# Performance work log

Measured on AMD Instinct MI355X. Metric: run time of the kernel, lower is better.

## Reference

```python
import jax, jax.numpy as jnp
import numpy as np

NEG_INF = -9e15  # matches the torch fill value


def setup_inputs() -> dict:
    key = jax.random.key(0)
    k1, k2, k3 = jax.random.split(key, 3)
    N, IN_F, OUT_F, C = 8192, 512, 64, 2
    x = jax.random.normal(k1, (N, IN_F), dtype=jnp.float32)
    W = jax.random.normal(k2, (OUT_F, IN_F), dtype=jnp.float32) * (1.0 / np.sqrt(IN_F))
    attention_raw = jax.random.normal(k3, (C * N, N), dtype=jnp.float32)
    return {"x": x, "W": W, "attention_raw": attention_raw, "k": 32}


def reference(x, W, attention_raw, k):
    # h = self.linear(input), bias=False
    h = x @ W.T  # [N, OUT_F]
    N, OUT_F = x.shape[0], W.shape[0]
    R = attention_raw.shape[0]  # C * N
    C = R // N

    # torch.topk(attention, k, dim=1); fill_(-9e15); scatter_ topk values back
    vals, idx = jax.lax.top_k(attention_raw, k)  # [R, k]
    rows = jnp.arange(R)[:, None]
    att = jnp.full_like(attention_raw, NEG_INF).at[rows, idx].set(vals)

    # row softmax; masked entries underflow to exactly 0 -> k-sparse rows
    att = jax.nn.softmax(att, axis=1)
    # dropout skipped (eval mode / deterministic reference)

    # spmm(nzidx, att[nzidx], N*C, N, h) == att @ h (zeros contribute nothing)
    h_prime = att @ h  # [C*N, OUT_F]

    # concat=True path: [C, N, F] -> [N, C, F] -> [N, C*F]
    out = h_prime.reshape(C, N, OUT_F).transpose(1, 0, 2).reshape(N, C * OUT_F)
    return out, att
```

## Files before the change

kernel.cpp:

```cpp
#include <hip/hip_runtime.h>

typedef unsigned int uint;
typedef unsigned short u16;
typedef unsigned long long u64;
typedef float v4f __attribute__((ext_vector_type(4)));

#define N_NODES 8192
#define IN_F    512
#define OUT_F   64
#define CHEADS  2
#define ROWS    (N_NODES * CHEADS)
#define ROW_LEN N_NODES
#define BLK     256
#define PER_TH  (ROW_LEN / BLK)
#define VCHUNKS (PER_TH / 4)
#define CAND_CAP 2048
#define SEL_CAP  64

__device__ __forceinline__ float bits_to_float(uint u) {
    union { uint u; float f; } cv; cv.u = u; return cv.f;
}
__device__ __forceinline__ uint float_to_bits(float f) {
    union { uint u; float f; } cv; cv.f = f; return cv.u;
}
__device__ __forceinline__ uint sortable32(uint u) {
    return u ^ ((u & 0x80000000u) ? 0xFFFFFFFFu : 0x80000000u);
}
__device__ __forceinline__ uint unsortable32(uint s) {
    return (s & 0x80000000u) ? (s ^ 0x80000000u) : ~s;
}
__device__ __forceinline__ float key_to_val(uint key) {
    return bits_to_float(unsortable32(key));
}

__device__ __forceinline__ int decode_k(const void* p) {
    int ki = *(const int*)p;
    if (ki >= 1 && ki <= ROW_LEN) return ki;
    {
        uint b = *(const u16*)p;
        float f = bits_to_float(b << 16);
        int kf = (int)f;
        if (f == (float)kf && kf >= 1 && kf <= ROW_LEN) return kf;
    }
    {
        float g = *(const float*)p;
        int kg = (int)g;
        if (g == (float)kg && kg >= 1 && kg <= ROW_LEN) return kg;
    }
    return 32;
}

__device__ __forceinline__ uint bitonic_desc_u32(uint v, const int lane) {
    #pragma unroll
    for (int size = 2; size <= 64; size <<= 1) {
        #pragma unroll
        for (int stride = size >> 1; stride > 0; stride >>= 1) {
            const uint pv = (uint)__shfl_xor((int)v, stride, 64);
            const bool takeMax = (((lane & stride) != 0) == ((lane & size) != 0));
            v = takeMax ? (v >= pv ? v : pv) : (v <= pv ? v : pv);
        }
    }
    return v;
}

__device__ __forceinline__ u64 bitonic_desc_u64(u64 v, const int lane) {
    #pragma unroll
    for (int size = 2; size <= 64; size <<= 1) {
        #pragma unroll
        for (int stride = size >> 1; stride > 0; stride >>= 1) {
            const u64 pv = __shfl_xor(v, stride, 64);
            const bool takeMax = (((lane & stride) != 0) == ((lane & size) != 0));
            v = takeMax ? (v >= pv ? v : pv) : (v <= pv ? v : pv);
        }
    }
    return v;
}

#define HM    32
#define HK    128
#define XS_LD 132

__global__ __launch_bounds__(256) void h_kernel(
    const float* __restrict__ x, const float* __restrict__ W, float* __restrict__ hbuf)
{
    __shared__ float x_s[HM * XS_LD];
    __shared__ float w_s[OUT_F * XS_LD];
    const int tid = threadIdx.x;
    const int n0  = blockIdx.x * HM;
    const int r   = tid & 15;
    const int fb  = (tid >> 4) << 2;

    float a00 = 0.f, a01 = 0.f, a02 = 0.f, a03 = 0.f;
    float a10 = 0.f, a11 = 0.f, a12 = 0.f, a13 = 0.f;

    for (int c = 0; c < IN_F; c += HK) {
        #pragma unroll
        for (int j = 0; j < 4; ++j) {
            const int id  = tid + 256 * j;
            const int row = id >> 5;
            const int c4  = id & 31;
            float4 v = *reinterpret_cast<const float4*>(x + (size_t)(n0 + row) * IN_F + c + 4 * c4);
            *reinterpret_cast<float4*>(&x_s[row * XS_LD + 4 * c4]) = v;
        }
        #pragma unroll
        for (int j = 0; j < 8; ++j) {
            const int id  = tid + 256 * j;
            const int row = id >> 5;
            const int c4  = id & 31;
            float4 v = *reinterpret_cast<const float4*>(W + (size_t)row * IN_F + c + 4 * c4);
            *reinterpret_cast<float4*>(&w_s[row * XS_LD + 4 * c4]) = v;
        }
        __syncthreads();

        #pragma unroll 4
        for (int k4 = 0; k4 < HK / 4; ++k4) {
            const float4 x0 = *reinterpret_cast<const float4*>(&x_s[r * XS_LD + 4 * k4]);
            const float4 x1 = *reinterpret_cast<const float4*>(&x_s[(r + 16) * XS_LD + 4 * k4]);
            const float4 w0 = *reinterpret_cast<const float4*>(&w_s[(fb + 0) * XS_LD + 4 * k4]);
            const float4 w1 = *reinterpret_cast<const float4*>(&w_s[(fb + 1) * XS_LD + 4 * k4]);
            const float4 w2 = *reinterpret_cast<const float4*>(&w_s[(fb + 2) * XS_LD + 4 * k4]);
            const float4 w3 = *reinterpret_cast<const float4*>(&w_s[(fb + 3) * XS_LD + 4 * k4]);
            a00 = fmaf(x0.x, w0.x, a00); a00 = fmaf(x0.y, w0.y, a00); a00 = fmaf(x0.z, w0.z, a00); a00 = fmaf(x0.w, w0.w, a00);
            a01 = fmaf(x0.x, w1.x, a01); a01 = fmaf(x0.y, w1.y, a01); a01 = fmaf(x0.z, w1.z, a01); a01 = fmaf(x0.w, w1.w, a01);
            a02 = fmaf(x0.x, w2.x, a02); a02 = fmaf(x0.y, w2.y, a02); a02 = fmaf(x0.z, w2.z, a02); a02 = fmaf(x0.w, w2.w, a02);
            a03 = fmaf(x0.x, w3.x, a03); a03 = fmaf(x0.y, w3.y, a03); a03 = fmaf(x0.z, w3.z, a03); a03 = fmaf(x0.w, w3.w, a03);
            a10 = fmaf(x1.x, w0.x, a10); a10 = fmaf(x1.y, w0.y, a10); a10 = fmaf(x1.z, w0.z, a10); a10 = fmaf(x1.w, w0.w, a10);
            a11 = fmaf(x1.x, w1.x, a11); a11 = fmaf(x1.y, w1.y, a11); a11 = fmaf(x1.z, w1.z, a11); a11 = fmaf(x1.w, w1.w, a11);
            a12 = fmaf(x1.x, w2.x, a12); a12 = fmaf(x1.y, w2.y, a12); a12 = fmaf(x1.z, w2.z, a12); a12 = fmaf(x1.w, w2.w, a12);
            a13 = fmaf(x1.x, w3.x, a13); a13 = fmaf(x1.y, w3.y, a13); a13 = fmaf(x1.z, w3.z, a13); a13 = fmaf(x1.w, w3.w, a13);
        }
        __syncthreads();
    }

    float4 o0; o0.x = a00; o0.y = a01; o0.z = a02; o0.w = a03;
    float4 o1; o1.x = a10; o1.y = a11; o1.z = a12; o1.w = a13;
    *reinterpret_cast<float4*>(hbuf + (size_t)(n0 + r) * OUT_F + fb)      = o0;
    *reinterpret_cast<float4*>(hbuf + (size_t)(n0 + r + 16) * OUT_F + fb) = o1;
}

__global__ __launch_bounds__(BLK) void topk_kernel(
    const float* __restrict__ attn,
    const float* __restrict__ hbuf,
    const void* __restrict__ kptr,
    float* __restrict__ outp,
    float* __restrict__ att_out)
{
    __shared__ uint  s_lmax[BLK];
    __shared__ uint  s_ck[CAND_CAP];
    __shared__ u16   s_cidx[CAND_CAP];
    __shared__ int   s_sel_idx[SEL_CAP];
    __shared__ float s_sel_w[SEL_CAP];
    __shared__ float s_lsum[4];
    __shared__ uint  s_bc[4];
    __shared__ int   s_cnt[2];
    __shared__ float s_l;
    __shared__ int   s_scnt;

    const int tid = threadIdx.x;
    const int row = blockIdx.x;
    int k = decode_k(kptr);
    if (k > SEL_CAP) k = SEL_CAP;

    if (tid == 0) { s_cnt[0] = 0; s_cnt[1] = 0; }

    const float* rowp = attn    + (size_t)row * ROW_LEN;
    float*       orow = att_out + (size_t)row * ROW_LEN;

    uint lk[PER_TH];
    uint lmax = 0;
    #pragma unroll
    for (int c = 0; c < VCHUNKS; ++c) {
        const int base = (c * BLK + tid) * 4;
        float4 v = *reinterpret_cast<const float4*>(rowp + base);
        const uint k0 = sortable32(float_to_bits(v.x));
        const uint k1 = sortable32(float_to_bits(v.y));
        const uint k2 = sortable32(float_to_bits(v.z));
        const uint k3 = sortable32(float_to_bits(v.w));
        lk[c * 4 + 0] = k0; lk[c * 4 + 1] = k1;
        lk[c * 4 + 2] = k2; lk[c * 4 + 3] = k3;
        lmax = max(max(max(lmax, k0), max(k1, k2)), k3);
    }
    s_lmax[tid] = lmax;
    __syncthreads();

    if (tid < 64) {
        uint cmb = max(max(s_lmax[tid], s_lmax[tid + 64]),
                       max(s_lmax[tid + 128], s_lmax[tid + 192]));
        cmb = bitonic_desc_u32(cmb, tid);
        const uint pk = (uint)__shfl((int)cmb, k - 1, 64);
        if (tid == 0) { s_bc[0] = pk; s_bc[1] = cmb; }
    } else {
        const int t = tid - 64;
        v4f z = {0.f, 0.f, 0.f, 0.f};
        for (int i = t; i < ROW_LEN / 4; i += 192)
            __builtin_nontemporal_store(z, reinterpret_cast<v4f*>(orow) + i);
    }
    __syncthreads();
    const uint  p = s_bc[0];
    const float m = key_to_val(s_bc[1]);

    #pragma unroll
    for (int e = 0; e < PER_TH; ++e) {
        if (lk[e] >= p) {
            int pos = atomicAdd(&s_cnt[0], 1);
            if (pos < CAND_CAP) {
                const int c = e >> 2, j = e & 3;
                s_ck[pos]   = lk[e];
                s_cidx[pos] = (u16)((c * BLK + tid) * 4 + j);
            }
        }
    }
    __syncthreads();

    int cnt = s_cnt[0];
    if (cnt > CAND_CAP) cnt = CAND_CAP;
    const bool fast = (cnt <= 64);

    if (fast) {
        if (tid < 64) {
            u64 v = 0ull;
            if (tid < cnt)
                v = ((u64)s_ck[tid] << 13) | (u64)(0x1FFFu ^ (uint)s_cidx[tid]);
            v = bitonic_desc_u64(v, tid);
            const uint key = (uint)(v >> 13);
            const int  idx = (int)(0x1FFFu ^ (uint)(v & 0x1FFFull));
            const float w  = (tid < k) ? __expf(key_to_val(key) - m) : 0.f;
            float lsum = w;
            #pragma unroll
            for (int off = 1; off < 64; off <<= 1) lsum += __shfl_xor(lsum, off, 64);
            if (tid < k) { s_sel_idx[tid] = idx; s_sel_w[tid] = w; }
            if (tid == 0) { s_l = lsum; s_scnt = k; }
        }
        __syncthreads();
    } else {
        if (tid < 64) {
            uint lo = p, hi = 0xFFFFFFFFu;
            while (lo < hi) {
                const uint d = hi - lo;
                const uint mid = lo + (d >> 1) + (d & 1u);
                int c = 0;
                for (int j = tid; j < cnt; j += 64) c += (s_ck[j] >= mid) ? 1 : 0;
                #pragma unroll
                for (int off = 1; off < 64; off <<= 1) c += __shfl_xor(c, off, 64);
                if (c >= k) lo = mid; else hi = mid - 1;
            }
            const uint V32 = lo;
            int g = 0;
            for (int j = tid; j < cnt; j += 64) g += (s_ck[j] > V32) ? 1 : 0;
            #pragma unroll
            for (int off = 1; off < 64; off <<= 1) g += __shfl_xor(g, off, 64);
            const int e_need = k - g;
            uint tlo = 0u, thi = 0x1FFFu;
            while (tlo < thi) {
                const uint d = thi - tlo;
                const uint mid = tlo + (d >> 1) + (d & 1u);
                int c = 0;
                for (int j = tid; j < cnt; j += 64)
                    c += (s_ck[j] == V32 && (0x1FFFu ^ (uint)s_cidx[j]) >= mid) ? 1 : 0;
                #pragma unroll
                for (int off = 1; off < 64; off <<= 1) c += __shfl_xor(c, off, 64);
                if (c >= e_need) tlo = mid; else thi = mid - 1;
            }
            if (tid == 0) { s_bc[2] = V32; s_bc[3] = tlo; }
        }
        __syncthreads();
        const uint V32  = s_bc[2];
        const uint Tlow = s_bc[3];
        float lsum = 0.f;
        #pragma unroll
        for (int e = 0; e < PER_TH; ++e) {
            const int idx = ((e >> 2) * BLK + tid) * 4 + (e & 3);
            const bool sel = (lk[e] > V32) || (lk[e] == V32 && (0x1FFFu ^ (uint)idx) >= Tlow);
            if (sel) {
                const float w = __expf(key_to_val(lk[e]) - m);
                lsum += w;
                int pos = atomicAdd(&s_cnt[1], 1);
                if (pos < SEL_CAP) { s_sel_idx[pos] = idx; s_sel_w[pos] = w; }
            }
        }
        #pragma unroll
        for (int off = 1; off < 64; off <<= 1) lsum += __shfl_xor(lsum, off, 64);
        if ((tid & 63) == 0) s_lsum[tid >> 6] = lsum;
        __syncthreads();
        if (tid == 0) {
            s_l = s_lsum[0] + s_lsum[1] + s_lsum[2] + s_lsum[3];
            int sc = s_cnt[1]; if (sc > SEL_CAP) sc = SEL_CAP;
            s_scnt = sc;
        }
        __syncthreads();
    }

    const float l     = s_l;
    const float inv_l = (l > 0.f) ? (1.0f / l) : 0.f;
    const int   scnt  = s_scnt;

    if (tid >= 64 && tid < 64 + scnt) {
        const int j = tid - 64;
        orow[s_sel_idx[j]] = s_sel_w[j] * inv_l;
    }

    const int n  = row & (N_NODES - 1);
    const int ch = row >> 13;
    if (tid < OUT_F) {
        float acc = 0.f;
        for (int j = 0; j < scnt; ++j)
            acc += s_sel_w[j] * hbuf[(size_t)s_sel_idx[j] * OUT_F + tid];
        outp[(size_t)n * (CHEADS * OUT_F) + ch * OUT_F + tid] = acc * inv_l;
    }
}

extern "C" void kernel_launch(void* const* d_in, const int* in_sizes, int n_in,
                              void* d_out, int out_size, void* d_ws, size_t ws_size,
                              hipStream_t stream) {
    const float* x    = (const float*)d_in[0];
    const float* W    = (const float*)d_in[1];
    const float* attn = (const float*)d_in[2];
    const void*  kptr = (const void*)d_in[3];

    float* hbuf = (float*)d_ws;
    float* outp = (float*)d_out;
    float* att_out = outp + (size_t)N_NODES * (CHEADS * OUT_F);

    hipLaunchKernelGGL(h_kernel,    dim3(N_NODES / HM), dim3(BLK), 0, stream, x, W, hbuf);
    hipLaunchKernelGGL(topk_kernel, dim3(ROWS),         dim3(BLK), 0, stream, attn, hbuf, kptr, outp, att_out);
}
```

Measured before the change: 915.8 us.

## Defer zero-fill of attention row to overlap with SpMM and use nontemporal loads

The zero-fill of each output attention row moves from the early phase, where it ran alongside the wave doing the bitonic threshold search, to the end of the kernel. There it runs in parallel with the 64 threads computing the h-weighted accumulation, followed by a barrier and the scatter of the selected softmax values. Row loads of the raw attention matrix now use nontemporal loads to avoid polluting cache. The h_kernel also remaps output columns to a strided pattern, and its unroll factor drops. Together these add an extra barrier and change the store coalescing in h_kernel.

```diff
diff --git a/kernel.cpp b/kernel.cpp
--- a/kernel.cpp
+++ b/kernel.cpp
@@ -88,7 +88,7 @@
     const int tid = threadIdx.x;
     const int n0  = blockIdx.x * HM;
     const int r   = tid & 15;
-    const int fb  = (tid >> 4) << 2;
+    const int cb  = tid >> 4;
 
     float a00 = 0.f, a01 = 0.f, a02 = 0.f, a03 = 0.f;
     float a10 = 0.f, a11 = 0.f, a12 = 0.f, a13 = 0.f;
@@ -112,14 +112,14 @@
         }
         __syncthreads();
 
-        #pragma unroll 4
+        #pragma unroll 2
         for (int k4 = 0; k4 < HK / 4; ++k4) {
             const float4 x0 = *reinterpret_cast<const float4*>(&x_s[r * XS_LD + 4 * k4]);
             const float4 x1 = *reinterpret_cast<const float4*>(&x_s[(r + 16) * XS_LD + 4 * k4]);
-            const float4 w0 = *reinterpret_cast<const float4*>(&w_s[(fb + 0) * XS_LD + 4 * k4]);
-            const float4 w1 = *reinterpret_cast<const float4*>(&w_s[(fb + 1) * XS_LD + 4 * k4]);
-            const float4 w2 = *reinterpret_cast<const float4*>(&w_s[(fb + 2) * XS_LD + 4 * k4]);
-            const float4 w3 = *reinterpret_cast<const float4*>(&w_s[(fb + 3) * XS_LD + 4 * k4]);
+            const float4 w0 = *reinterpret_cast<const float4*>(&w_s[(cb +  0) * XS_LD + 4 * k4]);
+            const float4 w1 = *reinterpret_cast<const float4*>(&w_s[(cb + 16) * XS_LD + 4 * k4]);
+            const float4 w2 = *reinterpret_cast<const float4*>(&w_s[(cb + 32) * XS_LD + 4 * k4]);
+            const float4 w3 = *reinterpret_cast<const float4*>(&w_s[(cb + 48) * XS_LD + 4 * k4]);
             a00 = fmaf(x0.x, w0.x, a00); a00 = fmaf(x0.y, w0.y, a00); a00 = fmaf(x0.z, w0.z, a00); a00 = fmaf(x0.w, w0.w, a00);
             a01 = fmaf(x0.x, w1.x, a01); a01 = fmaf(x0.y, w1.y, a01); a01 = fmaf(x0.z, w1.z, a01); a01 = fmaf(x0.w, w1.w, a01);
             a02 = fmaf(x0.x, w2.x, a02); a02 = fmaf(x0.y, w2.y, a02); a02 = fmaf(x0.z, w2.z, a02); a02 = fmaf(x0.w, w2.w, a02);
@@ -132,10 +132,10 @@
         __syncthreads();
     }
 
-    float4 o0; o0.x = a00; o0.y = a01; o0.z = a02; o0.w = a03;
-    float4 o1; o1.x = a10; o1.y = a11; o1.z = a12; o1.w = a13;
-    *reinterpret_cast<float4*>(hbuf + (size_t)(n0 + r) * OUT_F + fb)      = o0;
-    *reinterpret_cast<float4*>(hbuf + (size_t)(n0 + r + 16) * OUT_F + fb) = o1;
+    float* o0 = hbuf + (size_t)(n0 + r) * OUT_F + cb;
+    float* o1 = hbuf + (size_t)(n0 + r + 16) * OUT_F + cb;
+    o0[0] = a00; o0[16] = a01; o0[32] = a02; o0[48] = a03;
+    o1[0] = a10; o1[16] = a11; o1[32] = a12; o1[48] = a13;
 }
 
 __global__ __launch_bounds__(BLK) void topk_kernel(
@@ -170,12 +170,12 @@
     uint lmax = 0;
     #pragma unroll
     for (int c = 0; c < VCHUNKS; ++c) {
-        const int base = (c * BLK + tid) * 4;
-        float4 v = *reinterpret_cast<const float4*>(rowp + base);
-        const uint k0 = sortable32(float_to_bits(v.x));
-        const uint k1 = sortable32(float_to_bits(v.y));
-        const uint k2 = sortable32(float_to_bits(v.z));
-        const uint k3 = sortable32(float_to_bits(v.w));
+        const int vi = c * BLK + tid;
+        v4f v = __builtin_nontemporal_load(reinterpret_cast<const v4f*>(rowp) + vi);
+        const uint k0 = sortable32(float_to_bits(v[0]));
+        const uint k1 = sortable32(float_to_bits(v[1]));
+        const uint k2 = sortable32(float_to_bits(v[2]));
+        const uint k3 = sortable32(float_to_bits(v[3]));
         lk[c * 4 + 0] = k0; lk[c * 4 + 1] = k1;
         lk[c * 4 + 2] = k2; lk[c * 4 + 3] = k3;
         lmax = max(max(max(lmax, k0), max(k1, k2)), k3);
@@ -189,11 +189,6 @@
         cmb = bitonic_desc_u32(cmb, tid);
         const uint pk = (uint)__shfl((int)cmb, k - 1, 64);
         if (tid == 0) { s_bc[0] = pk; s_bc[1] = cmb; }
-    } else {
-        const int t = tid - 64;
-        v4f z = {0.f, 0.f, 0.f, 0.f};
-        for (int i = t; i < ROW_LEN / 4; i += 192)
-            __builtin_nontemporal_store(z, reinterpret_cast<v4f*>(orow) + i);
     }
     __syncthreads();
     const uint  p = s_bc[0];
@@ -294,11 +289,6 @@
     const float inv_l = (l > 0.f) ? (1.0f / l) : 0.f;
     const int   scnt  = s_scnt;
 
-    if (tid >= 64 && tid < 64 + scnt) {
-        const int j = tid - 64;
-        orow[s_sel_idx[j]] = s_sel_w[j] * inv_l;
-    }
-
     const int n  = row & (N_NODES - 1);
     const int ch = row >> 13;
     if (tid < OUT_F) {
@@ -306,7 +296,16 @@
         for (int j = 0; j < scnt; ++j)
             acc += s_sel_w[j] * hbuf[(size_t)s_sel_idx[j] * OUT_F + tid];
         outp[(size_t)n * (CHEADS * OUT_F) + ch * OUT_F + tid] = acc * inv_l;
-    }
+    } else {
+        const int t = tid - 64;
+        v4f z = {0.f, 0.f, 0.f, 0.f};
+        for (int i = t; i < ROW_LEN / 4; i += 192)
+            __builtin_nontemporal_store(z, reinterpret_cast<v4f*>(orow) + i);
+    }
+    __syncthreads();
+
+    if (tid < scnt)
+        orow[s_sel_idx[tid]] = s_sel_w[tid] * inv_l;
 }
 
 extern "C" void kernel_launch(void* const* d_in, const int* in_sizes, int n_in,
```

New measurement: 895.3 us. 1.02x faster.
